# Kernel optimization log

Measured on AMD Instinct MI355X. Metric: run time of the kernel, lower is better.

## Reference

```python
import jax, jax.numpy as jnp
import numpy as np

B, N, E, H = 16, 768, 1024, 16  # batch == heads so mask[i] (head-indexed, as in the source) is valid
D = E // H
MASK_P = 0.1
NEG = jnp.float32(-1e16)


def setup_inputs() -> dict:
    key = jax.random.key(0)
    ks = jax.random.split(key, 8)
    query = jax.random.normal(ks[0], (B, N, E), jnp.float32)
    key_t = jax.random.normal(ks[1], (B, N, E), jnp.float32)
    value = jax.random.normal(ks[2], (B, N, E), jnp.float32)
    u = jax.random.uniform(ks[3], (B, N))
    mask = jnp.where(u < MASK_P, -jnp.inf, 0.0).astype(jnp.float32)
    # per-head Linear(head_dim, head_dim, bias=False) weights, stacked over heads: (H, out=D, in=D)
    Wq = jax.random.normal(ks[4], (H, D, D), jnp.float32) * (1.0 / np.sqrt(D))
    Wk = jax.random.normal(ks[5], (H, D, D), jnp.float32) * (1.0 / np.sqrt(D))
    Wv = jax.random.normal(ks[6], (H, D, D), jnp.float32) * (1.0 / np.sqrt(D))
    Wf = jax.random.normal(ks[7], (E, E), jnp.float32) * (1.0 / np.sqrt(E))
    return {"query": query, "key": key_t, "value": value, "mask": mask,
            "Wq": Wq, "Wk": Wk, "Wv": Wv, "Wf": Wf}


def reference(query, key, value, mask, Wq, Wk, Wv, Wf):
    b, n, e = query.shape
    h = Wq.shape[0]
    d = e // h
    q = query.reshape(b, n, h, d)
    k = key.reshape(b, n, h, d)
    v = value.reshape(b, n, h, d)
    # per-head nn.Linear: x @ W[i].T  (W: (H, out, in))
    qh = jnp.einsum('bnhd,hed->bnhe', q, Wq)
    kh = jnp.einsum('bnhd,hed->bnhe', k, Wk)
    vh = jnp.einsum('bnhd,hed->bnhe', v, Wv)
    # scaled QK^T: divide by embed_size**0.5 (NOT head_dim) as in the source
    scores = jnp.einsum('bqhd,bkhd->bhqk', qh, kh) / jnp.sqrt(jnp.float32(e))  # (B,H,N,N)
    # faithful quirk: mask row selected by HEAD index i -> same additive mask for all batches
    bad = jnp.isneginf(mask)[:h]                      # (H, N)
    add = jnp.where(bad[:, :, None] | bad[:, None, :], NEG, jnp.float32(0.0))  # (H,N,N): row/col blanked
    probs = jax.nn.softmax(scores + add[None], axis=-1)
    attn = jnp.einsum('bhqk,bkhd->bqhd', probs, vh)   # (B,N,H,D)
    out = attn.reshape(b, n, e) @ Wf.T
    return out
```

## Files before the change

kernel.cpp:

```cpp
#include <hip/hip_runtime.h>

#define B_ 16
#define N_ 768
#define E_ 1024
#define H_ 16
#define D_ 64

typedef __bf16 bf16x8 __attribute__((ext_vector_type(8)));
typedef float f32x4 __attribute__((ext_vector_type(4)));
typedef unsigned short ushort8 __attribute__((ext_vector_type(8)));
typedef unsigned short ushort4v __attribute__((ext_vector_type(4)));
typedef unsigned int uint2v __attribute__((ext_vector_type(2)));
typedef unsigned int uint4v __attribute__((ext_vector_type(4)));

__device__ __forceinline__ unsigned short f2bf(float x) {
  unsigned u = __builtin_bit_cast(unsigned, x);
  u += 0x7FFFu + ((u >> 16) & 1u);
  return (unsigned short)(u >> 16);
}

__device__ __forceinline__ unsigned cvtpk(float lo, float hi) {
  unsigned r;
  asm("v_cvt_pk_bf16_f32 %0, %1, %2" : "=v"(r) : "v"(lo), "v"(hi));
  return r;
}

__device__ __forceinline__ float fexp2(float x) {
  float r;
  asm("v_exp_f32 %0, %1" : "=v"(r) : "v"(x));
  return r;
}

__device__ __forceinline__ f32x4 mfma16(ushort8 a, ushort8 b, f32x4 c) {
  return __builtin_amdgcn_mfma_f32_16x16x32_bf16(
      __builtin_bit_cast(bf16x8, a), __builtin_bit_cast(bf16x8, b), c, 0, 0, 0);
}

__global__ __launch_bounds__(256, 1) void proj_kernel(
    const float* __restrict__ q, const float* __restrict__ k, const float* __restrict__ v,
    const float* __restrict__ Wq, const float* __restrict__ Wk, const float* __restrict__ Wv,
    const float* __restrict__ Wf, unsigned short* __restrict__ Qh,
    unsigned short* __restrict__ Kh, unsigned short* __restrict__ Vt,
    unsigned short* __restrict__ Wfb) {
  const int m = blockIdx.x / 3072;
  const int rest = blockIdx.x - m * 3072;
  const int nt = rest % 12;
  const int bh = rest / 12;
  const int b = bh >> 4, h = bh & 15;
  const int tid = threadIdx.x;
  const int w = tid >> 6, l = tid & 63;
  const int l16 = l & 15, lg = l >> 4;

  __shared__ __align__(16) unsigned short Xs[64][72];
  __shared__ __align__(16) unsigned short Ws[64][72];

  const float* xp = (m == 0) ? q : (m == 1) ? k : v;
  const float* wp = ((m == 0) ? Wq : (m == 1) ? Wk : Wv) + (size_t)h * 4096;

  const int row = tid >> 4;
  const int c4 = (tid & 15) * 4;

  float4 xt[4], wt[4];
#pragma unroll
  for (int i = 0; i < 4; ++i)
    xt[i] = *(const float4*)&xp[((size_t)(b * N_ + nt * 64 + i * 16 + row)) * E_ + h * 64 + c4];
#pragma unroll
  for (int i = 0; i < 4; ++i)
    wt[i] = *(const float4*)&wp[(i * 16 + row) * 64 + c4];

  float4 wfv;
  if (blockIdx.x < 1024)
    wfv = *(const float4*)&Wf[((size_t)blockIdx.x * 256 + tid) * 4];

#pragma unroll
  for (int i = 0; i < 4; ++i) {
    ushort4v s;
    s[0] = f2bf(xt[i].x); s[1] = f2bf(xt[i].y); s[2] = f2bf(xt[i].z); s[3] = f2bf(xt[i].w);
    *(ushort4v*)&Xs[i * 16 + row][c4] = s;
  }
#pragma unroll
  for (int i = 0; i < 4; ++i) {
    ushort4v s;
    s[0] = f2bf(wt[i].x); s[1] = f2bf(wt[i].y); s[2] = f2bf(wt[i].z); s[3] = f2bf(wt[i].w);
    *(ushort4v*)&Ws[i * 16 + row][c4] = s;
  }
  if (blockIdx.x < 1024) {
    ushort4v s;
    s[0] = f2bf(wfv.x); s[1] = f2bf(wfv.y); s[2] = f2bf(wfv.z); s[3] = f2bf(wfv.w);
    *(ushort4v*)&Wfb[((size_t)blockIdx.x * 256 + tid) * 4] = s;
  }
  __syncthreads();

  f32x4 acc[4] = {};
#pragma unroll
  for (int kc = 0; kc < 2; ++kc) {
    ushort8 a = *(const ushort8*)&Xs[w * 16 + l16][kc * 32 + lg * 8];
#pragma unroll
    for (int eg = 0; eg < 4; ++eg) {
      ushort8 bf = *(const ushort8*)&Ws[eg * 16 + l16][kc * 32 + lg * 8];
      acc[eg] = mfma16(a, bf, acc[eg]);
    }
  }

  if (m < 2) {
    unsigned short* op = (m == 0) ? Qh : Kh;
    __syncthreads();
#pragma unroll
    for (int eg = 0; eg < 4; ++eg)
#pragma unroll
      for (int r = 0; r < 4; ++r)
        Xs[w * 16 + lg * 4 + r][eg * 16 + l16] = f2bf(acc[eg][r]);
    __syncthreads();
#pragma unroll
    for (int i = 0; i < 2; ++i) {
      int rw = i * 32 + (tid >> 3), c8 = (tid & 7) * 8;
      *(ushort8*)&op[((size_t)(b * H_ + h) * N_ + nt * 64 + rw) * 64 + c8] =
          *(const ushort8*)&Xs[rw][c8];
    }
  } else {
    __syncthreads();
#pragma unroll
    for (int eg = 0; eg < 4; ++eg) {
      uint2v pk;
      pk[0] = cvtpk(acc[eg][0], acc[eg][1]);
      pk[1] = cvtpk(acc[eg][2], acc[eg][3]);
      *(uint2v*)&Xs[eg * 16 + l16][w * 16 + lg * 4] = pk;
    }
    __syncthreads();
#pragma unroll
    for (int i = 0; i < 2; ++i) {
      int rw = i * 32 + (tid >> 3), c8 = (tid & 7) * 8;
      *(ushort8*)&Vt[((size_t)bh * 64 + rw) * N_ + nt * 64 + c8] =
          *(const ushort8*)&Xs[rw][c8];
    }
  }
}

__global__ __launch_bounds__(256, 4) void attn_kernel(
    const unsigned short* __restrict__ Qh, const unsigned short* __restrict__ Kh,
    const unsigned short* __restrict__ Vt, const float* __restrict__ mask,
    unsigned short* __restrict__ attnO) {
  const int bid = blockIdx.x;
  const int logical = (bid & 7) * 192 + (bid >> 3);
  const int qt = logical % 6;
  const int bh = logical / 6;
  const int b = bh >> 4, h = bh & 15;
  const int tid = threadIdx.x;
  const int w = tid >> 6, l = tid & 63;
  const int l16 = l & 15, lg = l >> 4;

  __shared__ __align__(16) unsigned short Ks[64][72];
  __shared__ __align__(16) unsigned short Vs[64][72];
  __shared__ float addk[N_];

  const size_t baseK = (size_t)bh * N_ * 64;
  const size_t baseV = (size_t)bh * 64 * N_;
  const int qrow0 = qt * 128 + w * 32;
  const float C2 = 0.04508422f;

  for (int i = tid; i < N_; i += 256)
    addk[i] = (mask[h * N_ + i] < -1e30f) ? -1.0e20f : 0.0f;

  ushort8 bQ[2][2];
#pragma unroll
  for (int qs = 0; qs < 2; ++qs)
#pragma unroll
    for (int kc = 0; kc < 2; ++kc)
      bQ[qs][kc] = *(const ushort8*)&Qh[((size_t)bh * N_ + qrow0 + qs * 16 + l16) * 64 +
                                        kc * 32 + lg * 8];
  float bqf[2];
#pragma unroll
  for (int qs = 0; qs < 2; ++qs)
    bqf[qs] = (mask[h * N_ + qrow0 + qs * 16 + l16] < -1e30f) ? 1.f : 0.f;

  const int srow = tid >> 3;
  const int sc8 = (tid & 7) * 8;

  uint4v kreg[2], vreg[2];
#pragma unroll
  for (int i = 0; i < 2; ++i) {
    int row = i * 32 + srow;
    kreg[i] = *(const uint4v*)&Kh[baseK + (size_t)row * 64 + sc8];
    vreg[i] = *(const uint4v*)&Vt[baseV + (size_t)row * N_ + sc8];
  }
  __syncthreads();
#pragma unroll
  for (int i = 0; i < 2; ++i) {
    int row = i * 32 + srow;
    *(ushort8*)&Ks[row][sc8] = __builtin_bit_cast(ushort8, kreg[i]);
    *(ushort8*)&Vs[row][sc8] = __builtin_bit_cast(ushort8, vreg[i]);
  }
  __syncthreads();

  f32x4 oacc[2][4] = {};
  float l_part[2] = {0.f, 0.f};

  for (int kt = 0; kt < 12; ++kt) {
    if (kt < 11) {
#pragma unroll
      for (int i = 0; i < 2; ++i) {
        int row = i * 32 + srow;
        kreg[i] = *(const uint4v*)&Kh[baseK + (size_t)((kt + 1) * 64 + row) * 64 + sc8];
        vreg[i] = *(const uint4v*)&Vt[baseV + (size_t)row * N_ + (kt + 1) * 64 + sc8];
      }
    }

    f32x4 st[4][2] = {};
#pragma unroll
    for (int kc = 0; kc < 2; ++kc) {
#pragma unroll
      for (int cg = 0; cg < 4; ++cg) {
        ushort8 aK = *(const ushort8*)&Ks[cg * 16 + l16][kc * 32 + lg * 8];
        st[cg][0] = mfma16(aK, bQ[0][kc], st[cg][0]);
        st[cg][1] = mfma16(aK, bQ[1][kc], st[cg][1]);
      }
    }

#pragma unroll
    for (int cg = 0; cg < 4; ++cg) {
      f32x4 ak4 = *(const f32x4*)&addk[kt * 64 + cg * 16 + lg * 4];
#pragma unroll
      for (int qs = 0; qs < 2; ++qs) {
#pragma unroll
        for (int r = 0; r < 4; ++r) {
          float t = __builtin_fmaf(st[cg][qs][r], C2, ak4[r]);
          t = (bqf[qs] > 0.f) ? 0.0f : t;
          float p = fexp2(t);
          l_part[qs] += p;
          st[cg][qs][r] = p;
        }
      }
    }

#pragma unroll
    for (int kcP = 0; kcP < 2; ++kcP) {
      ushort8 pa[2];
#pragma unroll
      for (int qs = 0; qs < 2; ++qs) {
        unsigned a0 = cvtpk(st[2 * kcP][qs][0], st[2 * kcP][qs][1]);
        unsigned b0 = cvtpk(st[2 * kcP][qs][2], st[2 * kcP][qs][3]);
        unsigned a1 = cvtpk(st[2 * kcP + 1][qs][0], st[2 * kcP + 1][qs][1]);
        unsigned b1 = cvtpk(st[2 * kcP + 1][qs][2], st[2 * kcP + 1][qs][3]);
        asm("v_permlane32_swap_b32 %0, %1" : "+v"(a0), "+v"(a1));
        asm("v_permlane16_swap_b32 %0, %1" : "+v"(a0), "+v"(a1));
        asm("v_permlane32_swap_b32 %0, %1" : "+v"(b0), "+v"(b1));
        asm("v_permlane16_swap_b32 %0, %1" : "+v"(b0), "+v"(b1));
        uint4v pk;
        pk[0] = a0; pk[1] = b0; pk[2] = a1; pk[3] = b1;
        pa[qs] = __builtin_bit_cast(ushort8, pk);
      }
#pragma unroll
      for (int dg = 0; dg < 4; ++dg) {
        ushort8 bv = *(const ushort8*)&Vs[dg * 16 + l16][kcP * 32 + lg * 8];
        oacc[0][dg] = mfma16(pa[0], bv, oacc[0][dg]);
        oacc[1][dg] = mfma16(pa[1], bv, oacc[1][dg]);
      }
    }

    __syncthreads();
    if (kt < 11) {
#pragma unroll
      for (int i = 0; i < 2; ++i) {
        int row = i * 32 + srow;
        *(ushort8*)&Ks[row][sc8] = __builtin_bit_cast(ushort8, kreg[i]);
        *(ushort8*)&Vs[row][sc8] = __builtin_bit_cast(ushort8, vreg[i]);
      }
    }
    __syncthreads();
  }

#pragma unroll
  for (int qs = 0; qs < 2; ++qs) {
    float s = l_part[qs];
    s += __shfl_xor(s, 16);
    s += __shfl_xor(s, 32);
#pragma unroll
    for (int r = 0; r < 4; ++r) {
      float dnm = __shfl(s, lg * 4 + r);
      float inv = 1.f / dnm;
      int qg = qrow0 + qs * 16 + lg * 4 + r;
      size_t orow = ((size_t)b * N_ + qg) * E_ + h * 64;
#pragma unroll
      for (int dg = 0; dg < 4; ++dg)
        attnO[orow + dg * 16 + l16] = f2bf(oacc[qs][dg][r] * inv);
    }
  }
}

__global__ __launch_bounds__(256) void gemm_kernel(const unsigned short* __restrict__ A,
                                                   const unsigned short* __restrict__ Bm,
                                                   float* __restrict__ out) {
  const int be = blockIdx.x & 7;
  const int bm = blockIdx.x >> 3;
  const int tid = threadIdx.x;
  const int w = tid >> 6, l = tid & 63;
  const int l16 = l & 15, lg = l >> 4;
  const int wm = w >> 1, wn = w & 1;

  __shared__ __align__(16) unsigned short As[128][72];
  __shared__ __align__(16) unsigned short Bs[128][72];

  f32x4 acc[4][4] = {};
  const int m0 = bm * 128, e0 = be * 128;
  const int srow = tid >> 3, sc8 = (tid & 7) * 8;
  const unsigned short* Ab = A + (size_t)(m0 + srow) * E_ + sc8;
  const unsigned short* Bb = Bm + (size_t)(e0 + srow) * E_ + sc8;

  uint4v ar[4], br[4];
#pragma unroll
  for (int i = 0; i < 4; ++i) {
    ar[i] = *(const uint4v*)(Ab + (size_t)i * 32 * E_);
    br[i] = *(const uint4v*)(Bb + (size_t)i * 32 * E_);
  }

  for (int kk = 0; kk < 16; ++kk) {
    __syncthreads();
#pragma unroll
    for (int i = 0; i < 4; ++i) {
      *(ushort8*)&As[i * 32 + srow][sc8] = __builtin_bit_cast(ushort8, ar[i]);
      *(ushort8*)&Bs[i * 32 + srow][sc8] = __builtin_bit_cast(ushort8, br[i]);
    }
    __syncthreads();
    if (kk < 15) {
#pragma unroll
      for (int i = 0; i < 4; ++i) {
        ar[i] = *(const uint4v*)(Ab + (size_t)i * 32 * E_ + (kk + 1) * 64);
        br[i] = *(const uint4v*)(Bb + (size_t)i * 32 * E_ + (kk + 1) * 64);
      }
    }
#pragma unroll
    for (int kc = 0; kc < 2; ++kc) {
      ushort8 a[4], bf[4];
#pragma unroll
      for (int i = 0; i < 4; ++i)
        a[i] = *(const ushort8*)&As[wm * 64 + i * 16 + l16][kc * 32 + lg * 8];
#pragma unroll
      for (int j = 0; j < 4; ++j)
        bf[j] = *(const ushort8*)&Bs[wn * 64 + j * 16 + l16][kc * 32 + lg * 8];
#pragma unroll
      for (int i = 0; i < 4; ++i)
#pragma unroll
        for (int j = 0; j < 4; ++j) acc[i][j] = mfma16(a[i], bf[j], acc[i][j]);
    }
  }

#pragma unroll
  for (int i = 0; i < 4; ++i)
#pragma unroll
    for (int j = 0; j < 4; ++j)
#pragma unroll
      for (int r = 0; r < 4; ++r)
        out[(size_t)(m0 + wm * 64 + i * 16 + lg * 4 + r) * E_ + e0 + wn * 64 + j * 16 + l16] =
            acc[i][j][r];
}

extern "C" void kernel_launch(void* const* d_in, const int* in_sizes, int n_in,
                              void* d_out, int out_size, void* d_ws, size_t ws_size,
                              hipStream_t stream) {
  const float* q = (const float*)d_in[0];
  const float* k = (const float*)d_in[1];
  const float* v = (const float*)d_in[2];
  const float* mask = (const float*)d_in[3];
  const float* Wq = (const float*)d_in[4];
  const float* Wk = (const float*)d_in[5];
  const float* Wv = (const float*)d_in[6];
  const float* Wf = (const float*)d_in[7];
  float* out = (float*)d_out;

  const size_t PH = (size_t)B_ * H_ * N_ * D_;
  unsigned short* Qh = (unsigned short*)d_ws;
  unsigned short* Kh = Qh + PH;
  unsigned short* Vt = Kh + PH;
  unsigned short* attn = Vt + PH;
  unsigned short* Wfb = attn + PH;

  proj_kernel<<<3 * B_ * H_ * (N_ / 64), 256, 0, stream>>>(q, k, v, Wq, Wk, Wv, Wf, Qh, Kh,
                                                           Vt, Wfb);
  attn_kernel<<<B_ * H_ * (N_ / 128), 256, 0, stream>>>(Qh, Kh, Vt, mask, attn);
  gemm_kernel<<<(B_ * N_ / 128) * (E_ / 128), 256, 0, stream>>>(attn, Wfb, out);
}
```

Baseline: 136.6 us.

## Process four row tiles per projection block with register prefetch of next tile

The projection kernel now loops over four consecutive 64-row tiles per block instead of one. The per-head weight tile is loaded into LDS once and reused across all four tiles. The next X tile is loaded into registers while the current tile's MFMAs run, and a separate output LDS buffer removes one barrier per tile. The trade is a 4x smaller grid (fewer blocks to hide memory latency with) and a launch-bounds hint raised to 2 blocks per CU.

Measured after the change: 135.6 us. No clear change (-0.7%).

```diff
diff --git a/kernel.cpp b/kernel.cpp
--- a/kernel.cpp
+++ b/kernel.cpp
@@ -36,48 +36,45 @@
       __builtin_bit_cast(bf16x8, a), __builtin_bit_cast(bf16x8, b), c, 0, 0, 0);
 }
 
-__global__ __launch_bounds__(256, 1) void proj_kernel(
+__global__ __launch_bounds__(256, 2) void proj_kernel(
     const float* __restrict__ q, const float* __restrict__ k, const float* __restrict__ v,
     const float* __restrict__ Wq, const float* __restrict__ Wk, const float* __restrict__ Wv,
     const float* __restrict__ Wf, unsigned short* __restrict__ Qh,
     unsigned short* __restrict__ Kh, unsigned short* __restrict__ Vt,
     unsigned short* __restrict__ Wfb) {
-  const int m = blockIdx.x / 3072;
-  const int rest = blockIdx.x - m * 3072;
-  const int nt = rest % 12;
-  const int bh = rest / 12;
+  const int m = blockIdx.x / 768;
+  const int rest = blockIdx.x - m * 768;
+  const int ng = rest % 3;
+  const int bh = rest / 3;
   const int b = bh >> 4, h = bh & 15;
+  const int nt0 = ng * 4;
   const int tid = threadIdx.x;
   const int w = tid >> 6, l = tid & 63;
   const int l16 = l & 15, lg = l >> 4;
 
   __shared__ __align__(16) unsigned short Xs[64][72];
   __shared__ __align__(16) unsigned short Ws[64][72];
+  __shared__ __align__(16) unsigned short Os[64][72];
 
   const float* xp = (m == 0) ? q : (m == 1) ? k : v;
   const float* wp = ((m == 0) ? Wq : (m == 1) ? Wk : Wv) + (size_t)h * 4096;
+  unsigned short* op = (m == 0) ? Qh : Kh;
 
   const int row = tid >> 4;
   const int c4 = (tid & 15) * 4;
 
-  float4 xt[4], wt[4];
-#pragma unroll
-  for (int i = 0; i < 4; ++i)
-    xt[i] = *(const float4*)&xp[((size_t)(b * N_ + nt * 64 + i * 16 + row)) * E_ + h * 64 + c4];
+  float4 wt[4], xt[4];
 #pragma unroll
   for (int i = 0; i < 4; ++i)
     wt[i] = *(const float4*)&wp[(i * 16 + row) * 64 + c4];
+#pragma unroll
+  for (int i = 0; i < 4; ++i)
+    xt[i] = *(const float4*)&xp[((size_t)(b * N_ + nt0 * 64 + i * 16 + row)) * E_ + h * 64 + c4];
 
   float4 wfv;
   if (blockIdx.x < 1024)
     wfv = *(const float4*)&Wf[((size_t)blockIdx.x * 256 + tid) * 4];
 
-#pragma unroll
-  for (int i = 0; i < 4; ++i) {
-    ushort4v s;
-    s[0] = f2bf(xt[i].x); s[1] = f2bf(xt[i].y); s[2] = f2bf(xt[i].z); s[3] = f2bf(xt[i].w);
-    *(ushort4v*)&Xs[i * 16 + row][c4] = s;
-  }
 #pragma unroll
   for (int i = 0; i < 4; ++i) {
     ushort4v s;
@@ -89,49 +86,65 @@
     s[0] = f2bf(wfv.x); s[1] = f2bf(wfv.y); s[2] = f2bf(wfv.z); s[3] = f2bf(wfv.w);
     *(ushort4v*)&Wfb[((size_t)blockIdx.x * 256 + tid) * 4] = s;
   }
-  __syncthreads();
-
-  f32x4 acc[4] = {};
-#pragma unroll
-  for (int kc = 0; kc < 2; ++kc) {
-    ushort8 a = *(const ushort8*)&Xs[w * 16 + l16][kc * 32 + lg * 8];
-#pragma unroll
-    for (int eg = 0; eg < 4; ++eg) {
-      ushort8 bf = *(const ushort8*)&Ws[eg * 16 + l16][kc * 32 + lg * 8];
-      acc[eg] = mfma16(a, bf, acc[eg]);
-    }
-  }
-
-  if (m < 2) {
-    unsigned short* op = (m == 0) ? Qh : Kh;
-    __syncthreads();
-#pragma unroll
-    for (int eg = 0; eg < 4; ++eg)
-#pragma unroll
-      for (int r = 0; r < 4; ++r)
-        Xs[w * 16 + lg * 4 + r][eg * 16 + l16] = f2bf(acc[eg][r]);
-    __syncthreads();
-#pragma unroll
-    for (int i = 0; i < 2; ++i) {
-      int rw = i * 32 + (tid >> 3), c8 = (tid & 7) * 8;
-      *(ushort8*)&op[((size_t)(b * H_ + h) * N_ + nt * 64 + rw) * 64 + c8] =
-          *(const ushort8*)&Xs[rw][c8];
-    }
-  } else {
-    __syncthreads();
-#pragma unroll
-    for (int eg = 0; eg < 4; ++eg) {
-      uint2v pk;
-      pk[0] = cvtpk(acc[eg][0], acc[eg][1]);
-      pk[1] = cvtpk(acc[eg][2], acc[eg][3]);
-      *(uint2v*)&Xs[eg * 16 + l16][w * 16 + lg * 4] = pk;
-    }
-    __syncthreads();
-#pragma unroll
-    for (int i = 0; i < 2; ++i) {
-      int rw = i * 32 + (tid >> 3), c8 = (tid & 7) * 8;
-      *(ushort8*)&Vt[((size_t)bh * 64 + rw) * N_ + nt * 64 + c8] =
-          *(const ushort8*)&Xs[rw][c8];
+
+  for (int t = 0; t < 4; ++t) {
+#pragma unroll
+    for (int i = 0; i < 4; ++i) {
+      ushort4v s;
+      s[0] = f2bf(xt[i].x); s[1] = f2bf(xt[i].y); s[2] = f2bf(xt[i].z); s[3] = f2bf(xt[i].w);
+      *(ushort4v*)&Xs[i * 16 + row][c4] = s;
+    }
+    __syncthreads();
+
+    if (t < 3) {
+#pragma unroll
+      for (int i = 0; i < 4; ++i)
+        xt[i] = *(const float4*)&xp[((size_t)(b * N_ + (nt0 + t + 1) * 64 + i * 16 + row)) * E_ +
+                                    h * 64 + c4];
+    }
+
+    f32x4 acc[4] = {};
+#pragma unroll
+    for (int kc = 0; kc < 2; ++kc) {
+      ushort8 a = *(const ushort8*)&Xs[w * 16 + l16][kc * 32 + lg * 8];
+#pragma unroll
+      for (int eg = 0; eg < 4; ++eg) {
+        ushort8 bf = *(const ushort8*)&Ws[eg * 16 + l16][kc * 32 + lg * 8];
+        acc[eg] = mfma16(a, bf, acc[eg]);
+      }
+    }
+
+    if (m < 2) {
+#pragma unroll
+      for (int eg = 0; eg < 4; ++eg)
+#pragma unroll
+        for (int r = 0; r < 4; ++r)
+          Os[w * 16 + lg * 4 + r][eg * 16 + l16] = f2bf(acc[eg][r]);
+    } else {
+#pragma unroll
+      for (int eg = 0; eg < 4; ++eg) {
+        uint2v pk;
+        pk[0] = cvtpk(acc[eg][0], acc[eg][1]);
+        pk[1] = cvtpk(acc[eg][2], acc[eg][3]);
+        *(uint2v*)&Os[eg * 16 + l16][w * 16 + lg * 4] = pk;
+      }
+    }
+    __syncthreads();
+
+    if (m < 2) {
+#pragma unroll
+      for (int i = 0; i < 2; ++i) {
+        int rw = i * 32 + (tid >> 3), c8 = (tid & 7) * 8;
+        *(ushort8*)&op[((size_t)(b * H_ + h) * N_ + (nt0 + t) * 64 + rw) * 64 + c8] =
+            *(const ushort8*)&Os[rw][c8];
+      }
+    } else {
+#pragma unroll
+      for (int i = 0; i < 2; ++i) {
+        int rw = i * 32 + (tid >> 3), c8 = (tid & 7) * 8;
+        *(ushort8*)&Vt[((size_t)bh * 64 + rw) * N_ + (nt0 + t) * 64 + c8] =
+            *(const ushort8*)&Os[rw][c8];
+      }
     }
   }
 }
@@ -374,8 +387,8 @@
   unsigned short* attn = Vt + PH;
   unsigned short* Wfb = attn + PH;
 
-  proj_kernel<<<3 * B_ * H_ * (N_ / 64), 256, 0, stream>>>(q, k, v, Wq, Wk, Wv, Wf, Qh, Kh,
-                                                           Vt, Wfb);
+  proj_kernel<<<3 * B_ * H_ * (N_ / 256), 256, 0, stream>>>(q, k, v, Wq, Wk, Wv, Wf, Qh, Kh,
+                                                            Vt, Wfb);
   attn_kernel<<<B_ * H_ * (N_ / 128), 256, 0, stream>>>(Qh, Kh, Vt, mask, attn);
   gemm_kernel<<<(B_ * N_ / 128) * (E_ / 128), 256, 0, stream>>>(attn, Wfb, out);
 }
```
